# Optimization experiments

Hardware: AMD Instinct MI355X
Metric: run time of the kernel (lower is better)

## Reference

```python
import jax, jax.numpy as jnp
import numpy as np

# QTIP QuantizedLinear config (decode_mode='lut')
IN_F, OUT_F = 4096, 4096
TD_X, TD_Y = 16, 16          # weight tile
L, K, V = 16, 2, 2           # trellis state bits, bits/weight, values/state
TLUT_BITS = 16               # lut mode: tlut_bits == L


def fwht(x):
    """Normalized fast Walsh-Hadamard transform over the last axis (power of 2).
    Equivalent to matmul_hadU with K=1 (features are powers of two)."""
    n = x.shape[-1]
    h = 1
    while h < n:
        x = x.reshape(x.shape[:-1] + (n // (2 * h), 2, h))
        a, b = x[..., 0, :], x[..., 1, :]
        x = jnp.stack([a + b, a - b], axis=-2).reshape(x.shape[:-3] + (n,))
        h *= 2
    return x / jnp.sqrt(jnp.float32(n))


def dequantize_weight(trellis, tlut):
    """Bitshift trellis decode: each 16x16 tile stores td_x*td_y*K = 512 bits.
    The stream is walked KV = K*V bits per step (tail-biting); each L-bit state
    indexes the LUT producing V weights. trellis holds uint16 words in int32."""
    num_tiles = trellis.shape[0]
    T = TD_X * TD_Y            # 256 weights per tile
    S = T // V                 # 128 trellis steps per tile
    KV = K * V                 # 4 fresh bits per step
    steps = L // KV            # 4 nibbles form one L-bit state
    words = trellis & 0xFFFF
    bit_pos = jnp.arange(15, -1, -1)                     # MSB-first within word
    bits = (words[:, :, None] >> bit_pos) & 1            # (tiles, 32, 16)
    nib_w = 2 ** jnp.arange(KV - 1, -1, -1)
    nibs = jnp.sum(bits.reshape(num_tiles, S, KV) * nib_w, axis=-1)  # (tiles, S)
    # state_i = (nib[i-3]<<12)|(nib[i-2]<<8)|(nib[i-1]<<4)|nib[i], wraparound (tail-biting)
    states = jnp.zeros_like(nibs)
    for j in range(steps):
        states = states | (jnp.roll(nibs, j, axis=1) << (KV * j))
    vals = tlut[states]                                  # (tiles, S, V)
    W = vals.reshape(OUT_F // TD_X, IN_F // TD_Y, TD_X, TD_Y)
    return W.transpose(0, 2, 1, 3).reshape(OUT_F, IN_F)


def setup_inputs() -> dict:
    key = jax.random.key(0)
    k1, k2, k3, k4, k5 = jax.random.split(key, 5)
    inp = jax.random.normal(k1, (8, 2048, IN_F), jnp.float32)
    num_tiles = (OUT_F // TD_X) * (IN_F // TD_Y)
    words = (TD_X * TD_Y * K + 15) // 16
    trellis = jax.random.randint(k2, (num_tiles, words), 0, 65536, jnp.int32)
    tlut = jax.random.normal(k3, (2 ** TLUT_BITS, V), jnp.float32)
    SU = jax.random.normal(k4, (IN_F,), jnp.float32)
    SV = jax.random.normal(k5, (OUT_F,), jnp.float32)
    return {"input": inp, "trellis": trellis, "tlut": tlut, "SU": SU, "SV": SV}


def reference(input, trellis, tlut, SU, SV):
    W = dequantize_weight(trellis, tlut)          # (OUT_F, IN_F)
    x = input.reshape(-1, IN_F) * SU              # input rescale (sign vector)
    x = fwht(x)                                   # left Hadamard rotation
    x = x @ W.T                                   # fused dequant matmul
    x = fwht(x)                                   # right Hadamard rotation
    x = x * SV                                    # output rescale
    return x.reshape(input.shape[:-1] + (OUT_F,))
```

## Files before the change

### kernel.cpp

```cpp
#include <hip/hip_runtime.h>

typedef __attribute__((ext_vector_type(8))) short short8;
typedef __attribute__((ext_vector_type(4))) float f32x4;

__device__ __forceinline__ unsigned short f2bf(float f) {
  union { float f; unsigned u; } x{f};
  unsigned r = x.u + 0x7FFFu + ((x.u >> 16) & 1u);
  return (unsigned short)(r >> 16);
}

__device__ __forceinline__ void gload_lds16(const void* g, void* l) {
  __builtin_amdgcn_global_load_lds(
      (__attribute__((address_space(1))) void*)((unsigned long long)g),
      (__attribute__((address_space(3))) void*)(unsigned)((unsigned long long)l),
      16, 0, 0);
}

__device__ __forceinline__ void butterfly64(float (*tile)[64], int t) {
  const int c  = t & 63;
  const int pb = t >> 6;
#pragma unroll
  for (int h = 1; h < 64; h <<= 1) {
#pragma unroll
    for (int k = 0; k < 8; ++k) {
      const int p  = pb + (k << 2);
      const int j1 = ((p & ~(h - 1)) << 1) | (p & (h - 1));
      const int j2 = j1 + h;
      const float a = tile[j1][c], b = tile[j2][c];
      tile[j1][c] = a + b;
      tile[j2][c] = a - b;
    }
    __syncthreads();
  }
}

__global__ void k_deq_col1(const int* __restrict__ trellis,
                           const float* __restrict__ tlut,
                           float* __restrict__ W) {
  __shared__ unsigned short words[16][32];
  __shared__ float tile[64][64];
  const int t  = threadIdx.x;
  const int rg = blockIdx.x >> 6;
  const int cg = blockIdx.x & 63;
#pragma unroll
  for (int r = 0; r < 2; ++r) {
    const int ff = t + (r << 8);
    const int a = ff >> 7, rw = ff & 127;
    const int src = ((rg * 4 + a) * 256 + cg * 4) * 32 + rw;
    ((unsigned short*)words)[a * 128 + rw] = (unsigned short)(trellis[src] & 0xFFFF);
  }
  __syncthreads();
#pragma unroll
  for (int r = 0; r < 8; ++r) {
    const int f  = t + (r << 8);
    const int tl = f >> 7, s = f & 127;
    const unsigned short* w = words[tl];
    unsigned state = 0;
#pragma unroll
    for (int j = 0; j < 4; ++j) {
      const int ss = (s - j) & 127;
      state |= (((unsigned)w[ss >> 2] >> (12 - 4 * (ss & 3))) & 0xFu) << (4 * j);
    }
    const float2 v = *(const float2*)(tlut + (size_t)state * 2);
    const int o = ((tl >> 2) << 4) + (s >> 3);
    const int i = ((tl & 3) << 4) + ((s & 7) << 1);
    tile[o][i]     = v.x;
    tile[o][i + 1] = v.y;
  }
  __syncthreads();
  butterfly64(tile, t);
  const size_t base = ((size_t)(rg * 64)) * 4096 + cg * 64;
#pragma unroll
  for (int k = 0; k < 4; ++k) {
    const int idx = t + (k << 8);
    const int r = idx >> 4, c4 = idx & 15;
    *(float4*)(W + base + (size_t)r * 4096 + (c4 << 2)) = *(float4*)(&tile[r][c4 << 2]);
  }
}

__global__ void k_fwht_row(float* __restrict__ W) {
  __shared__ float row[4096];
  const int t = threadIdx.x;
  float* g = W + ((size_t)blockIdx.x << 12);
#pragma unroll
  for (int k = 0; k < 4; ++k) {
    const int e = (t + (k << 8)) << 2;
    *(float4*)(row + e) = *(const float4*)(g + e);
  }
  __syncthreads();
  for (int h = 1; h < 4096; h <<= 1) {
#pragma unroll
    for (int k = 0; k < 8; ++k) {
      const int p  = t + (k << 8);
      const int j1 = ((p & ~(h - 1)) << 1) | (p & (h - 1));
      const int j2 = j1 + h;
      const float a = row[j1], b = row[j2];
      row[j1] = a + b;
      row[j2] = a - b;
    }
    __syncthreads();
  }
#pragma unroll
  for (int k = 0; k < 4; ++k) {
    const int e = (t + (k << 8)) << 2;
    float4 v = *(float4*)(row + e);
    v.x *= 0.015625f; v.y *= 0.015625f; v.z *= 0.015625f; v.w *= 0.015625f;
    *(float4*)(g + e) = v;
  }
}

__global__ void k_fwht_col2(const float* __restrict__ W,
                            const float* __restrict__ SU,
                            const float* __restrict__ SV,
                            unsigned short* __restrict__ Mt) {
  __shared__ float tile[64][64];
  const int t  = threadIdx.x;
  const int b  = blockIdx.x >> 6;
  const int cg = blockIdx.x & 63;
#pragma unroll
  for (int k = 0; k < 4; ++k) {
    const int idx = t + (k << 8);
    const int a = idx >> 4, c4 = idx & 15;
    const int row = (a << 6) + b;
    *(float4*)(&tile[a][c4 << 2]) =
        *(const float4*)(W + (size_t)row * 4096 + ((size_t)cg << 6) + (c4 << 2));
  }
  __syncthreads();
  butterfly64(tile, t);
#pragma unroll
  for (int k = 0; k < 4; ++k) {
    const int idx = t + (k << 8);
    const int a = idx >> 4, c4 = idx & 15;
    const int row = (a << 6) + b;
    const int col0 = (cg << 6) + (c4 << 2);
    const float sv = SV[row] * 0.015625f;
    const float4 su = *(const float4*)(SU + col0);
    const float4 v = *(float4*)(&tile[a][c4 << 2]);
    ushort4 o;
    o.x = f2bf(v.x * sv * su.x);
    o.y = f2bf(v.y * sv * su.y);
    o.z = f2bf(v.z * sv * su.z);
    o.w = f2bf(v.w * sv * su.w);
    *(ushort4*)(Mt + (size_t)row * 4096 + col0) = o;
  }
}

__global__ void k_cvt_x(const float* __restrict__ x, unsigned short* __restrict__ xb) {
  const long long n4 = (long long)16384 * 4096 / 4;
  long long i = (long long)blockIdx.x * blockDim.x + threadIdx.x;
  const long long stride = (long long)gridDim.x * blockDim.x;
  for (; i < n4; i += stride) {
    const float4 v = *(const float4*)(x + i * 4);
    ushort4 o;
    o.x = f2bf(v.x); o.y = f2bf(v.y); o.z = f2bf(v.z); o.w = f2bf(v.w);
    *(ushort4*)(xb + i * 4) = o;
  }
}

#define BARRIER __builtin_amdgcn_s_barrier()
#define WAITV4  asm volatile("s_waitcnt vmcnt(4)" ::: "memory")
#define WAITV0  asm volatile("s_waitcnt vmcnt(0)" ::: "memory")

#define STAGE_A(db, h, jj) do { \
  gload_lds16(aRow + (((size_t)((h)*128      )) << 12) + ((jj) << 6), smem +         (db)*32768 + (h)*16384 +        w1k); \
  gload_lds16(aRow + (((size_t)((h)*128 + 64 )) << 12) + ((jj) << 6), smem +         (db)*32768 + (h)*16384 + 8192 + w1k); \
} while (0)
#define STAGE_B(db, h, jj) do { \
  gload_lds16(bRow + (((size_t)((h)*128      )) << 12) + ((jj) << 6), smem + 65536 + (db)*32768 + (h)*16384 +        w1k); \
  gload_lds16(bRow + (((size_t)((h)*128 + 64 )) << 12) + ((jj) << 6), smem + 65536 + (db)*32768 + (h)*16384 + 8192 + w1k); \
} while (0)

#define RD_A(kk, base, cx) do { _Pragma("unroll") \
  for (int mi = 0; mi < 8; ++mi) af[mi][kk] = *(const short8*)((base) + mi*2048 + (cx)); } while (0)
#define RD_B(kk, base, cx) do { _Pragma("unroll") \
  for (int ni = 0; ni < 4; ++ni) bb[ni][kk] = *(const short8*)((base) + ni*2048 + (cx)); } while (0)

#define MMA(nA, nB, kk) do { _Pragma("unroll") \
  for (int mi = 0; mi < 8; ++mi) { \
    acc[mi][nA] = __builtin_amdgcn_mfma_f32_16x16x32_bf16(af[mi][kk], bb[nA][kk], acc[mi][nA], 0, 0, 0); \
    acc[mi][nB] = __builtin_amdgcn_mfma_f32_16x16x32_bf16(af[mi][kk], bb[nB][kk], acc[mi][nB], 0, 0, 0); \
  } } while (0)

#define PHASE(READS, STAGE, WAIT, MMAC) do { \
  READS; STAGE; WAIT; \
  BARRIER; \
  __builtin_amdgcn_s_setprio(1); MMAC; __builtin_amdgcn_s_setprio(0); \
  BARRIER; \
} while (0)

__global__ void __launch_bounds__(512, 2)
k_gemm8(const unsigned short* __restrict__ A,
        const unsigned short* __restrict__ B,
        float* __restrict__ C) {
  extern __shared__ char smem[];
  const int t    = threadIdx.x;
  const int lane = t & 63, w = t >> 6;
  const int wr   = w >> 2, wc = w & 3;
  const int hb   = wc >> 1, rb = (wc & 1) * 64;
  const int lr   = lane & 15, q = lane >> 4;
  const int w1k  = w * 1024;

  const int nt = blockIdx.x & 15;
  const int mt = blockIdx.x >> 4;

  const int cx0 = lr * 128 + (((0 + q) ^ (lr & 7)) << 4);
  const int cx1 = lr * 128 + (((4 + q) ^ (lr & 7)) << 4);

  const char* As0 = smem +         wr * 16384;
  const char* As1 = smem + 32768 + wr * 16384;
  const char* Bs0 = smem + 65536 +         hb * 16384 + rb * 128;
  const char* Bs1 = smem + 65536 + 32768 + hb * 16384 + rb * 128;

  const int srow  = t >> 3;
  const int csrc8 = (((t & 7) ^ (srow & 7)) << 3);
  const unsigned short* aRow = A + (((size_t)(mt * 256 + srow)) << 12) + csrc8;
  const unsigned short* bRow = B + (((size_t)(nt * 256 + srow)) << 12) + csrc8;

  short8 af[8][2], bb[4][2];
  f32x4  acc[8][4];
#pragma unroll
  for (int i = 0; i < 8; ++i)
#pragma unroll
    for (int j = 0; j < 4; ++j) acc[i][j] = (f32x4){0.f, 0.f, 0.f, 0.f};

  STAGE_A(0, 0, 0); STAGE_A(0, 1, 0); STAGE_B(0, 0, 0); STAGE_B(0, 1, 0);
  STAGE_A(1, 0, 1); STAGE_A(1, 1, 1);
  WAITV4;
  BARRIER;

  for (int g = 0; g < 31; ++g) {
    const int j1 = 2 * g + 1, j2 = 2 * g + 2, j3 = 2 * g + 3;
    PHASE({ RD_B(0, Bs0, cx0); RD_A(0, As0, cx0); }, STAGE_B(1, 0, j1), , MMA(0, 1, 0));
    PHASE({ RD_A(1, As0, cx1); },                    STAGE_B(1, 1, j1), , MMA(2, 3, 0));
    PHASE({ RD_B(1, Bs0, cx1); },                    STAGE_A(0, 0, j2), , MMA(0, 1, 1));
    PHASE({ },                                       STAGE_A(0, 1, j2), WAITV4, MMA(2, 3, 1));
    PHASE({ RD_B(0, Bs1, cx0); RD_A(0, As1, cx0); }, STAGE_B(0, 0, j2), , MMA(0, 1, 0));
    PHASE({ RD_A(1, As1, cx1); },                    STAGE_B(0, 1, j2), , MMA(2, 3, 0));
    PHASE({ RD_B(1, Bs1, cx1); },                    STAGE_A(1, 0, j3), , MMA(0, 1, 1));
    PHASE({ },                                       STAGE_A(1, 1, j3), WAITV4, MMA(2, 3, 1));
  }
  PHASE({ RD_B(0, Bs0, cx0); RD_A(0, As0, cx0); }, STAGE_B(1, 0, 63), , MMA(0, 1, 0));
  PHASE({ RD_A(1, As0, cx1); },                    STAGE_B(1, 1, 63), , MMA(2, 3, 0));
  PHASE({ RD_B(1, Bs0, cx1); },                    ,                   , MMA(0, 1, 1));
  PHASE({ },                                       ,                   WAITV0, MMA(2, 3, 1));
  PHASE({ RD_B(0, Bs1, cx0); RD_A(0, As1, cx0); }, ,                   , MMA(0, 1, 0));
  PHASE({ RD_A(1, As1, cx1); },                    ,                   , MMA(2, 3, 0));
  PHASE({ RD_B(1, Bs1, cx1); },                    ,                   , MMA(0, 1, 1));
  PHASE({ },                                       ,                   , MMA(2, 3, 1));

  float* cbase = C + (((size_t)(mt * 256 + wr * 128 + q * 4)) << 12)
               + nt * 256 + wc * 64 + lr;
#pragma unroll
  for (int mi = 0; mi < 8; ++mi)
#pragma unroll
    for (int ni = 0; ni < 4; ++ni)
#pragma unroll
      for (int r = 0; r < 4; ++r)
        cbase[(((size_t)(mi * 16 + r)) << 12) + ni * 16] = acc[mi][ni][r];
}

extern "C" void kernel_launch(void* const* d_in, const int* in_sizes, int n_in,
                              void* d_out, int out_size, void* d_ws, size_t ws_size,
                              hipStream_t stream) {
  const float* x       = (const float*)d_in[0];
  const int*   trellis = (const int*)d_in[1];
  const float* tlut    = (const float*)d_in[2];
  const float* SU      = (const float*)d_in[3];
  const float* SV      = (const float*)d_in[4];
  float* out = (float*)d_out;

  char* ws = (char*)d_ws;
  float*          W  = (float*)ws;
  unsigned short* Mt = (unsigned short*)(ws + (64ull << 20));
  unsigned short* xb = (unsigned short*)(ws + (96ull << 20));

  hipFuncSetAttribute(reinterpret_cast<const void*>(&k_gemm8),
                      hipFuncAttributeMaxDynamicSharedMemorySize, 131072);

  hipLaunchKernelGGL(k_deq_col1,  dim3(4096),  dim3(256), 0, stream, trellis, tlut, W);
  hipLaunchKernelGGL(k_fwht_row,  dim3(4096),  dim3(256), 0, stream, W);
  hipLaunchKernelGGL(k_fwht_col2, dim3(4096),  dim3(256), 0, stream, W, SU, SV, Mt);
  hipLaunchKernelGGL(k_cvt_x,     dim3(2048),  dim3(256), 0, stream, x, xb);
  hipLaunchKernelGGL(k_gemm8,     dim3(1024),  dim3(512), 131072, stream, xb, Mt, out);
}
```

Baseline: 614.1 us.

## Software-pipeline LDS fragment reads one phase ahead of MFMA in GEMM loop

Restructures the 8-phase GEMM main loop so each phase's LDS fragment reads feed a later phase's MFMAs instead of the current one. Register reads of A and B sub-fragments are split into B01/B23 halves and interleaved so reads overlap the preceding MFMA block. The vmcnt waits are moved earlier and loosened to vmcnt(2) to match the new staging order. This aims to hide LDS read latency behind matrix math, at the cost of more live registers and a more fragile barrier and wait ordering.

```diff
diff --git a/kernel.cpp b/kernel.cpp
--- a/kernel.cpp
+++ b/kernel.cpp
@@ -159,6 +159,7 @@
 
 #define BARRIER __builtin_amdgcn_s_barrier()
 #define WAITV4  asm volatile("s_waitcnt vmcnt(4)" ::: "memory")
+#define WAITV2  asm volatile("s_waitcnt vmcnt(2)" ::: "memory")
 #define WAITV0  asm volatile("s_waitcnt vmcnt(0)" ::: "memory")
 
 #define STAGE_A(db, h, jj) do { \
@@ -170,15 +171,24 @@
   gload_lds16(bRow + (((size_t)((h)*128 + 64 )) << 12) + ((jj) << 6), smem + 65536 + (db)*32768 + (h)*16384 + 8192 + w1k); \
 } while (0)
 
-#define RD_A(kk, base, cx) do { _Pragma("unroll") \
+#define RD_AF(kk, base, cx) do { _Pragma("unroll") \
   for (int mi = 0; mi < 8; ++mi) af[mi][kk] = *(const short8*)((base) + mi*2048 + (cx)); } while (0)
-#define RD_B(kk, base, cx) do { _Pragma("unroll") \
-  for (int ni = 0; ni < 4; ++ni) bb[ni][kk] = *(const short8*)((base) + ni*2048 + (cx)); } while (0)
-
-#define MMA(nA, nB, kk) do { _Pragma("unroll") \
+#define RD_B01(kk, base, cx) do { \
+  bb[0][kk] = *(const short8*)((base) + 0*2048 + (cx)); \
+  bb[1][kk] = *(const short8*)((base) + 1*2048 + (cx)); } while (0)
+#define RD_B23(kk, base, cx) do { \
+  bb[2][kk] = *(const short8*)((base) + 2*2048 + (cx)); \
+  bb[3][kk] = *(const short8*)((base) + 3*2048 + (cx)); } while (0)
+
+#define MMA01(kk) do { _Pragma("unroll") \
   for (int mi = 0; mi < 8; ++mi) { \
-    acc[mi][nA] = __builtin_amdgcn_mfma_f32_16x16x32_bf16(af[mi][kk], bb[nA][kk], acc[mi][nA], 0, 0, 0); \
-    acc[mi][nB] = __builtin_amdgcn_mfma_f32_16x16x32_bf16(af[mi][kk], bb[nB][kk], acc[mi][nB], 0, 0, 0); \
+    acc[mi][0] = __builtin_amdgcn_mfma_f32_16x16x32_bf16(af[mi][kk], bb[0][kk], acc[mi][0], 0, 0, 0); \
+    acc[mi][1] = __builtin_amdgcn_mfma_f32_16x16x32_bf16(af[mi][kk], bb[1][kk], acc[mi][1], 0, 0, 0); \
+  } } while (0)
+#define MMA23(kk) do { _Pragma("unroll") \
+  for (int mi = 0; mi < 8; ++mi) { \
+    acc[mi][2] = __builtin_amdgcn_mfma_f32_16x16x32_bf16(af[mi][kk], bb[2][kk], acc[mi][2], 0, 0, 0); \
+    acc[mi][3] = __builtin_amdgcn_mfma_f32_16x16x32_bf16(af[mi][kk], bb[3][kk], acc[mi][3], 0, 0, 0); \
   } } while (0)
 
 #define PHASE(READS, STAGE, WAIT, MMAC) do { \
@@ -227,26 +237,27 @@
   STAGE_A(1, 0, 1); STAGE_A(1, 1, 1);
   WAITV4;
   BARRIER;
+  RD_AF(0, As0, cx0); RD_B01(0, Bs0, cx0);
 
   for (int g = 0; g < 31; ++g) {
-    const int j1 = 2 * g + 1, j2 = 2 * g + 2, j3 = 2 * g + 3;
-    PHASE({ RD_B(0, Bs0, cx0); RD_A(0, As0, cx0); }, STAGE_B(1, 0, j1), , MMA(0, 1, 0));
-    PHASE({ RD_A(1, As0, cx1); },                    STAGE_B(1, 1, j1), , MMA(2, 3, 0));
-    PHASE({ RD_B(1, Bs0, cx1); },                    STAGE_A(0, 0, j2), , MMA(0, 1, 1));
-    PHASE({ },                                       STAGE_A(0, 1, j2), WAITV4, MMA(2, 3, 1));
-    PHASE({ RD_B(0, Bs1, cx0); RD_A(0, As1, cx0); }, STAGE_B(0, 0, j2), , MMA(0, 1, 0));
-    PHASE({ RD_A(1, As1, cx1); },                    STAGE_B(0, 1, j2), , MMA(2, 3, 0));
-    PHASE({ RD_B(1, Bs1, cx1); },                    STAGE_A(1, 0, j3), , MMA(0, 1, 1));
-    PHASE({ },                                       STAGE_A(1, 1, j3), WAITV4, MMA(2, 3, 1));
-  }
-  PHASE({ RD_B(0, Bs0, cx0); RD_A(0, As0, cx0); }, STAGE_B(1, 0, 63), , MMA(0, 1, 0));
-  PHASE({ RD_A(1, As0, cx1); },                    STAGE_B(1, 1, 63), , MMA(2, 3, 0));
-  PHASE({ RD_B(1, Bs0, cx1); },                    ,                   , MMA(0, 1, 1));
-  PHASE({ },                                       ,                   WAITV0, MMA(2, 3, 1));
-  PHASE({ RD_B(0, Bs1, cx0); RD_A(0, As1, cx0); }, ,                   , MMA(0, 1, 0));
-  PHASE({ RD_A(1, As1, cx1); },                    ,                   , MMA(2, 3, 0));
-  PHASE({ RD_B(1, Bs1, cx1); },                    ,                   , MMA(0, 1, 1));
-  PHASE({ },                                       ,                   , MMA(2, 3, 1));
+    const int jv = 2 * g + 1, ju2 = 2 * g + 2, jv2 = 2 * g + 3;
+    PHASE({ RD_B23(0, Bs0, cx0); },                    STAGE_B(1, 0, jv),  ,       MMA01(0));
+    PHASE({ RD_AF(1, As0, cx1); RD_B01(1, Bs0, cx1); },STAGE_B(1, 1, jv),  ,       MMA23(0));
+    PHASE({ RD_B23(1, Bs0, cx1); },                    STAGE_A(0, 0, ju2), WAITV2, MMA01(1));
+    PHASE({ RD_AF(0, As1, cx0); RD_B01(0, Bs1, cx0); },STAGE_A(0, 1, ju2), ,       MMA23(1));
+    PHASE({ RD_B23(0, Bs1, cx0); },                    STAGE_B(0, 0, ju2), ,       MMA01(0));
+    PHASE({ RD_AF(1, As1, cx1); RD_B01(1, Bs1, cx1); },STAGE_B(0, 1, ju2), ,       MMA23(0));
+    PHASE({ RD_B23(1, Bs1, cx1); },                    STAGE_A(1, 0, jv2), WAITV2, MMA01(1));
+    PHASE({ RD_AF(0, As0, cx0); RD_B01(0, Bs0, cx0); },STAGE_A(1, 1, jv2), ,       MMA23(1));
+  }
+  PHASE({ RD_B23(0, Bs0, cx0); },                    STAGE_B(1, 0, 63), ,       MMA01(0));
+  PHASE({ RD_AF(1, As0, cx1); RD_B01(1, Bs0, cx1); },STAGE_B(1, 1, 63), ,       MMA23(0));
+  PHASE({ RD_B23(1, Bs0, cx1); },                    ,                  WAITV0, MMA01(1));
+  PHASE({ RD_AF(0, As1, cx0); RD_B01(0, Bs1, cx0); },,                  ,       MMA23(1));
+  PHASE({ RD_B23(0, Bs1, cx0); },                    ,                  ,       MMA01(0));
+  PHASE({ RD_AF(1, As1, cx1); RD_B01(1, Bs1, cx1); },,                  ,       MMA23(0));
+  PHASE({ RD_B23(1, Bs1, cx1); },                    ,                  ,       MMA01(1));
+  PHASE({ },                                         ,                  ,       MMA23(1));
 
   float* cbase = C + (((size_t)(mt * 256 + wr * 128 + q * 4)) << 12)
                + nt * 256 + wc * 64 + lr;
```

After: 629.2 us. 2.5% more time.

## Replace 8-phase interleaved GEMM pipeline with simple per-k-tile double buffering

Applied to the files above, without the earlier changes.

Replaces the fine-grained eight-phase schedule, which interleaved partial LDS reads, partial global-to-LDS stages and half-MMAs with two barriers per phase, with one k-tile step. Each step waits for all loads, does a single barrier, issues all eight staging loads for the next tile, then runs both k-halves of MMAs. This removes many barriers and the complex phasing, but the full vmcnt(0) wait each tile exposes more load latency. The next tile's stage also writes the buffer that other waves may still be reading from the previous step, which may be a race.

```diff
diff --git a/kernel.cpp b/kernel.cpp
--- a/kernel.cpp
+++ b/kernel.cpp
@@ -158,34 +158,54 @@
 }
 
 #define BARRIER __builtin_amdgcn_s_barrier()
-#define WAITV4  asm volatile("s_waitcnt vmcnt(4)" ::: "memory")
 #define WAITV0  asm volatile("s_waitcnt vmcnt(0)" ::: "memory")
 
-#define STAGE_A(db, h, jj) do { \
-  gload_lds16(aRow + (((size_t)((h)*128      )) << 12) + ((jj) << 6), smem +         (db)*32768 + (h)*16384 +        w1k); \
-  gload_lds16(aRow + (((size_t)((h)*128 + 64 )) << 12) + ((jj) << 6), smem +         (db)*32768 + (h)*16384 + 8192 + w1k); \
-} while (0)
-#define STAGE_B(db, h, jj) do { \
-  gload_lds16(bRow + (((size_t)((h)*128      )) << 12) + ((jj) << 6), smem + 65536 + (db)*32768 + (h)*16384 +        w1k); \
-  gload_lds16(bRow + (((size_t)((h)*128 + 64 )) << 12) + ((jj) << 6), smem + 65536 + (db)*32768 + (h)*16384 + 8192 + w1k); \
-} while (0)
-
-#define RD_A(kk, base, cx) do { _Pragma("unroll") \
+#define STAGE_A(db, jj) do { \
+  gload_lds16(aRow,                      smem +         (db)*32768 +         w1k + ((size_t)(jj) << 6)*2); \
+  gload_lds16(aRow + ( 64ull << 12),     smem +         (db)*32768 +  8192 + w1k + ((size_t)(jj) << 6)*2); \
+  gload_lds16(aRow + (128ull << 12),     smem +         (db)*32768 + 16384 + w1k + ((size_t)(jj) << 6)*2); \
+  gload_lds16(aRow + (192ull << 12),     smem +         (db)*32768 + 24576 + w1k + ((size_t)(jj) << 6)*2); \
+} while (0)
+#define STAGE_B(db, jj) do { \
+  gload_lds16(bRow,                      smem + 65536 + (db)*32768 +         w1k + ((size_t)(jj) << 6)*2); \
+  gload_lds16(bRow + ( 64ull << 12),     smem + 65536 + (db)*32768 +  8192 + w1k + ((size_t)(jj) << 6)*2); \
+  gload_lds16(bRow + (128ull << 12),     smem + 65536 + (db)*32768 + 16384 + w1k + ((size_t)(jj) << 6)*2); \
+  gload_lds16(bRow + (192ull << 12),     smem + 65536 + (db)*32768 + 24576 + w1k + ((size_t)(jj) << 6)*2); \
+} while (0)
+
+#define RD_AF(kk, base, cx) do { _Pragma("unroll") \
   for (int mi = 0; mi < 8; ++mi) af[mi][kk] = *(const short8*)((base) + mi*2048 + (cx)); } while (0)
-#define RD_B(kk, base, cx) do { _Pragma("unroll") \
+#define RD_BB(kk, base, cx) do { _Pragma("unroll") \
   for (int ni = 0; ni < 4; ++ni) bb[ni][kk] = *(const short8*)((base) + ni*2048 + (cx)); } while (0)
 
-#define MMA(nA, nB, kk) do { _Pragma("unroll") \
+#define MMA_K(kk) do { _Pragma("unroll") \
   for (int mi = 0; mi < 8; ++mi) { \
-    acc[mi][nA] = __builtin_amdgcn_mfma_f32_16x16x32_bf16(af[mi][kk], bb[nA][kk], acc[mi][nA], 0, 0, 0); \
-    acc[mi][nB] = __builtin_amdgcn_mfma_f32_16x16x32_bf16(af[mi][kk], bb[nB][kk], acc[mi][nB], 0, 0, 0); \
+    acc[mi][0] = __builtin_amdgcn_mfma_f32_16x16x32_bf16(af[mi][kk], bb[0][kk], acc[mi][0], 0, 0, 0); \
+    acc[mi][1] = __builtin_amdgcn_mfma_f32_16x16x32_bf16(af[mi][kk], bb[1][kk], acc[mi][1], 0, 0, 0); \
+    acc[mi][2] = __builtin_amdgcn_mfma_f32_16x16x32_bf16(af[mi][kk], bb[2][kk], acc[mi][2], 0, 0, 0); \
+    acc[mi][3] = __builtin_amdgcn_mfma_f32_16x16x32_bf16(af[mi][kk], bb[3][kk], acc[mi][3], 0, 0, 0); \
   } } while (0)
 
-#define PHASE(READS, STAGE, WAIT, MMAC) do { \
-  READS; STAGE; WAIT; \
-  BARRIER; \
-  __builtin_amdgcn_s_setprio(1); MMAC; __builtin_amdgcn_s_setprio(0); \
-  BARRIER; \
+#define KTILE(Asx, Bsx, STAGES) do { \
+  WAITV0; BARRIER; \
+  STAGES; \
+  RD_BB(0, Bsx, cx0); RD_AF(0, Asx, cx0); \
+  __builtin_amdgcn_s_setprio(1); MMA_K(0); __builtin_amdgcn_s_setprio(0); \
+  RD_BB(1, Bsx, cx1); RD_AF(1, Asx, cx1); \
+  __builtin_amdgcn_s_setprio(1); MMA_K(1); __builtin_amdgcn_s_setprio(0); \
+} while (0)
+
+#define STAGE_ALL(db, jj) do { \
+  const unsigned short* aJ = aRow + ((jj) << 6); \
+  const unsigned short* bJ = bRow + ((jj) << 6); \
+  gload_lds16(aJ,                  smem +         (db)*32768 +         w1k); \
+  gload_lds16(aJ + ( 64ull << 12), smem +         (db)*32768 +  8192 + w1k); \
+  gload_lds16(aJ + (128ull << 12), smem +         (db)*32768 + 16384 + w1k); \
+  gload_lds16(aJ + (192ull << 12), smem +         (db)*32768 + 24576 + w1k); \
+  gload_lds16(bJ,                  smem + 65536 + (db)*32768 +         w1k); \
+  gload_lds16(bJ + ( 64ull << 12), smem + 65536 + (db)*32768 +  8192 + w1k); \
+  gload_lds16(bJ + (128ull << 12), smem + 65536 + (db)*32768 + 16384 + w1k); \
+  gload_lds16(bJ + (192ull << 12), smem + 65536 + (db)*32768 + 24576 + w1k); \
 } while (0)
 
 __global__ void __launch_bounds__(512, 2)
@@ -223,30 +243,14 @@
 #pragma unroll
     for (int j = 0; j < 4; ++j) acc[i][j] = (f32x4){0.f, 0.f, 0.f, 0.f};
 
-  STAGE_A(0, 0, 0); STAGE_A(0, 1, 0); STAGE_B(0, 0, 0); STAGE_B(0, 1, 0);
-  STAGE_A(1, 0, 1); STAGE_A(1, 1, 1);
-  WAITV4;
-  BARRIER;
+  STAGE_ALL(0, 0);
 
   for (int g = 0; g < 31; ++g) {
-    const int j1 = 2 * g + 1, j2 = 2 * g + 2, j3 = 2 * g + 3;
-    PHASE({ RD_B(0, Bs0, cx0); RD_A(0, As0, cx0); }, STAGE_B(1, 0, j1), , MMA(0, 1, 0));
-    PHASE({ RD_A(1, As0, cx1); },                    STAGE_B(1, 1, j1), , MMA(2, 3, 0));
-    PHASE({ RD_B(1, Bs0, cx1); },                    STAGE_A(0, 0, j2), , MMA(0, 1, 1));
-    PHASE({ },                                       STAGE_A(0, 1, j2), WAITV4, MMA(2, 3, 1));
-    PHASE({ RD_B(0, Bs1, cx0); RD_A(0, As1, cx0); }, STAGE_B(0, 0, j2), , MMA(0, 1, 0));
-    PHASE({ RD_A(1, As1, cx1); },                    STAGE_B(0, 1, j2), , MMA(2, 3, 0));
-    PHASE({ RD_B(1, Bs1, cx1); },                    STAGE_A(1, 0, j3), , MMA(0, 1, 1));
-    PHASE({ },                                       STAGE_A(1, 1, j3), WAITV4, MMA(2, 3, 1));
-  }
-  PHASE({ RD_B(0, Bs0, cx0); RD_A(0, As0, cx0); }, STAGE_B(1, 0, 63), , MMA(0, 1, 0));
-  PHASE({ RD_A(1, As0, cx1); },                    STAGE_B(1, 1, 63), , MMA(2, 3, 0));
-  PHASE({ RD_B(1, Bs0, cx1); },                    ,                   , MMA(0, 1, 1));
-  PHASE({ },                                       ,                   WAITV0, MMA(2, 3, 1));
-  PHASE({ RD_B(0, Bs1, cx0); RD_A(0, As1, cx0); }, ,                   , MMA(0, 1, 0));
-  PHASE({ RD_A(1, As1, cx1); },                    ,                   , MMA(2, 3, 0));
-  PHASE({ RD_B(1, Bs1, cx1); },                    ,                   , MMA(0, 1, 1));
-  PHASE({ },                                       ,                   , MMA(2, 3, 1));
+    KTILE(As0, Bs0, STAGE_ALL(1, 2 * g + 1));
+    KTILE(As1, Bs1, STAGE_ALL(0, 2 * g + 2));
+  }
+  KTILE(As0, Bs0, STAGE_ALL(1, 63));
+  KTILE(As1, Bs1, {});
 
   float* cbase = C + (((size_t)(mt * 256 + wr * 128 + q * 4)) << 12)
                + nt * 256 + wc * 64 + lr;
```

After: 622.2 us. Within noise of the previous version (+1.3%).
